# Optimization experiments

Measured on AMD Instinct MI355X. Metric: run time of the kernel, lower is better.

The kernel has to match this reference:

```python
import jax, jax.numpy as jnp
import numpy as np

T, B, IN, H, L = 512, 32, 320, 1024, 3
SLOPE, OFFSET = 0.2, 0.5
FORGET_BIAS = 1.0


def setup_inputs() -> dict:
    key = jax.random.key(0)
    ks = iter(jax.random.split(key, 64))
    stdv = 1.0 / np.sqrt(H)

    def u(k, shape):
        return jax.random.uniform(k, shape, jnp.float32, -stdv, stdv)

    inp = {
        "x": jax.random.normal(next(ks), (T, B, IN), jnp.float32),
        "h0": jnp.zeros((2 * L, B, H), jnp.float32),
        "c0": jnp.zeros((2 * L, B, H), jnp.float32),
    }
    for l in range(L):
        isz = IN if l == 0 else 2 * H
        for d in ("f", "r"):
            inp[f"w_ih_{l}{d}"] = u(next(ks), (4 * H, isz))
            inp[f"w_hh_{l}{d}"] = u(next(ks), (4 * H, H))
            b_ih = u(next(ks), (4 * H,))
            # forget_gate_bias: bias_ih forget slice set, bias_hh forget slice zeroed
            b_ih = b_ih.at[H:2 * H].set(FORGET_BIAS)
            b_hh = u(next(ks), (4 * H,))
            b_hh = b_hh.at[H:2 * H].set(0.0)
            inp[f"b_ih_{l}{d}"] = b_ih
            inp[f"b_hh_{l}{d}"] = b_hh
    return inp


def _hard_lstm_scan(x_seq, h, c, w_ih, w_hh, b):
    """x_seq: [T,B,I]; h,c: [B,H]. Returns ys [T,B,H], (h,c)."""
    # Batch the input-to-hidden GEMM across all timesteps.
    gx = jnp.einsum("tbi,gi->tbg", x_seq, w_ih) + b  # [T,B,4H]

    def step(carry, gxt):
        h, c = carry
        g = gxt + h @ w_hh.T
        i, f, gg, o = jnp.split(g, 4, axis=-1)
        i = jnp.clip(SLOPE * i + OFFSET, 0.0, 1.0)
        f = jnp.clip(SLOPE * f + OFFSET, 0.0, 1.0)
        gg = jnp.clip(gg, -1.0, 1.0)        # hardtanh
        o = jnp.clip(SLOPE * o + OFFSET, 0.0, 1.0)
        c = f * c + i * gg
        h = o * jnp.clip(c, -1.0, 1.0)
        return (h, c), h

    (h, c), ys = jax.lax.scan(step, (h, c), gx)
    return ys, h, c


def hard_lstm_forward(x, h0, c0, params):
    """params: list of L tuples ((fwd 4-tuple), (rev 4-tuple))."""
    y = x
    for l, (pf, pr) in enumerate(params):
        w_ih_f, w_hh_f, b_ih_f, b_hh_f = pf
        w_ih_r, w_hh_r, b_ih_r, b_hh_r = pr
        yf, _, _ = _hard_lstm_scan(y, h0[2 * l], c0[2 * l], w_ih_f, w_hh_f, b_ih_f + b_hh_f)
        yr, _, _ = _hard_lstm_scan(y[::-1], h0[2 * l + 1], c0[2 * l + 1], w_ih_r, w_hh_r, b_ih_r + b_hh_r)
        y = jnp.concatenate([yf, yr[::-1]], axis=-1)  # [T,B,2H]
    return y


def reference(x, h0, c0,
              w_ih_0f, w_hh_0f, b_ih_0f, b_hh_0f,
              w_ih_0r, w_hh_0r, b_ih_0r, b_hh_0r,
              w_ih_1f, w_hh_1f, b_ih_1f, b_hh_1f,
              w_ih_1r, w_hh_1r, b_ih_1r, b_hh_1r,
              w_ih_2f, w_hh_2f, b_ih_2f, b_hh_2f,
              w_ih_2r, w_hh_2r, b_ih_2r, b_hh_2r):
    params = [
        ((w_ih_0f, w_hh_0f, b_ih_0f, b_hh_0f), (w_ih_0r, w_hh_0r, b_ih_0r, b_hh_0r)),
        ((w_ih_1f, w_hh_1f, b_ih_1f, b_hh_1f), (w_ih_1r, w_hh_1r, b_ih_1r, b_hh_1r)),
        ((w_ih_2f, w_hh_2f, b_ih_2f, b_hh_2f), (w_ih_2r, w_hh_2r, b_ih_2r, b_hh_2r)),
    ]
    return hard_lstm_forward(x, h0, c0, params)
```

## Files before the change

kernel.cpp:

```cpp
#include <hip/hip_runtime.h>

typedef __attribute__((ext_vector_type(8))) short short8;
typedef __attribute__((ext_vector_type(4))) short short4v;
typedef __attribute__((ext_vector_type(4))) float f32x4;

__device__ __forceinline__ short f2bf(float x) {
  union { float f; unsigned u; } v; v.f = x;
  unsigned r = v.u + 0x7fffu + ((v.u >> 16) & 1u);
  return (short)(r >> 16);
}
__device__ __forceinline__ float bf2f(short b) {
  union { unsigned u; float f; } v; v.u = ((unsigned)(unsigned short)b) << 16;
  return v.f;
}

#define GLOAD_LDS16(g, l) __builtin_amdgcn_global_load_lds( \
    (const __attribute__((address_space(1))) void*)(g),     \
    (__attribute__((address_space(3))) void*)(l), 16, 0, 0)

__global__ void k_cvt(const float* __restrict__ s, short* __restrict__ d, int n) {
  int stride = gridDim.x * blockDim.x * 4;
  for (int i = (blockIdx.x * blockDim.x + threadIdx.x) * 4; i < n; i += stride) {
    float4 v = *(const float4*)(s + i);
    short4v o;
    o.x = f2bf(v.x); o.y = f2bf(v.y); o.z = f2bf(v.z); o.w = f2bf(v.w);
    *(short4v*)(d + i) = o;
  }
}

__global__ void k_bias(const float* __restrict__ bif, const float* __restrict__ bhf,
                       const float* __restrict__ bir, const float* __restrict__ bhr,
                       float* __restrict__ o) {
  int i = blockIdx.x * 256 + threadIdx.x;
  o[i] = (i < 4096) ? (bif[i] + bhf[i]) : (bir[i - 4096] + bhr[i - 4096]);
}

__global__ void k_zero(int* __restrict__ p) { p[blockIdx.x * 256 + threadIdx.x] = 0; }

__global__ void __launch_bounds__(256) k_gemm(
    const short* __restrict__ A, const short* __restrict__ Bt,
    const float* __restrict__ bias, short* __restrict__ C,
    int M, int N, int K)
{
  __shared__ short Al[128 * 64];
  __shared__ short Bl[128 * 64];
  const int nm = M >> 7;
  int wg = blockIdx.x;
  int q = gridDim.x >> 3;
  wg = (wg & 7) * q + (wg >> 3);
  const int mt = wg % nm, nt = wg / nm;
  const int tid = threadIdx.x, lane = tid & 63, w = tid >> 6;
  const int wr = w >> 1, wc = w & 1;
  const short* Ab = A + (size_t)(mt * 128) * K;
  const short* Bb = Bt + (size_t)(nt * 128) * K;
  f32x4 acc[4][4] = {};
  const int lrow = lane >> 3, lseg = lane & 7;

  for (int kt = 0; kt < K; kt += 64) {
#pragma unroll
    for (int s = 0; s < 4; ++s) {
      int chunk = s * 4 + w;
      int r = chunk * 8 + lrow;
      GLOAD_LDS16(Ab + (size_t)r * K + kt + lseg * 8, &Al[chunk * 512]);
      GLOAD_LDS16(Bb + (size_t)r * K + kt + lseg * 8, &Bl[chunk * 512]);
    }
    __syncthreads();
#pragma unroll
    for (int kk = 0; kk < 2; ++kk) {
      short8 af[4], bfr[4];
#pragma unroll
      for (int i = 0; i < 4; ++i) {
        af[i]  = *(const short8*)&Al[(wr * 64 + i * 16 + (lane & 15)) * 64 + kk * 32 + (lane >> 4) * 8];
        bfr[i] = *(const short8*)&Bl[(wc * 64 + i * 16 + (lane & 15)) * 64 + kk * 32 + (lane >> 4) * 8];
      }
#pragma unroll
      for (int i = 0; i < 4; ++i)
#pragma unroll
        for (int j = 0; j < 4; ++j)
          acc[i][j] = __builtin_amdgcn_mfma_f32_16x16x32_bf16(af[i], bfr[j], acc[i][j], 0, 0, 0);
    }
    __syncthreads();
  }

  const int r0 = mt * 128 + wr * 64, c0n = nt * 128 + wc * 64;
#pragma unroll
  for (int i = 0; i < 4; ++i) {
#pragma unroll
    for (int j = 0; j < 4; ++j) {
      int col = c0n + j * 16 + (lane & 15);
      float bv = bias[col];
#pragma unroll
      for (int r = 0; r < 4; ++r) {
        int row = r0 + i * 16 + (lane >> 4) * 4 + r;
        C[(size_t)row * N + col] = f2bf(acc[i][j][r] + bv);
      }
    }
  }
}

__device__ __forceinline__ void seqwait_slice(int* seqbase, int target, int kq, int lane) {
  if (lane < 32) {
    int* sp = seqbase + (kq * 32 + lane) * 32;
    while (__hip_atomic_load(sp, __ATOMIC_RELAXED, __HIP_MEMORY_SCOPE_AGENT) < target)
      __builtin_amdgcn_s_sleep(1);
  }
  asm volatile("" ::: "memory");
}

template <bool LAST>
__global__ void __launch_bounds__(256, 1) k_scan(
    const short* __restrict__ gx,
    const short* __restrict__ whh,
    const float* __restrict__ h0,
    const float* __restrict__ c0,
    short* __restrict__ hbuf,
    void* __restrict__ yout,
    int layer, int* __restrict__ bar)
{
  const int tid = threadIdx.x, lane = tid & 63, kq = tid >> 6;
  const int dir = blockIdx.x >> 7, wid = blockIdx.x & 127;
  const int hc0 = wid * 8;
  __shared__ float part[4][32][35];
  int* seq = bar + dir * 128 * 32;

  short8 wfr[16];
#pragma unroll
  for (int ni = 0; ni < 2; ++ni) {
    const int lcol = ni * 16 + (lane & 15);
    const int grow = dir * 4096 + (lcol >> 3) * 1024 + hc0 + (lcol & 7);
    const short* wp = whh + (size_t)grow * 1024 + kq * 256 + (lane >> 4) * 8;
#pragma unroll
    for (int ks = 0; ks < 8; ++ks) wfr[ni * 8 + ks] = *(const short8*)(wp + ks * 32);
  }
#pragma unroll
  for (int i = 0; i < 16; ++i) asm volatile("" : "+v"(wfr[i]));

  const int b4 = tid >> 1, cg = tid & 1, col0 = hc0 + cg * 4;
  float ca[4] = {0.f, 0.f, 0.f, 0.f};
  short4v pgi, pgf, pgg, pgo;
  if (tid < 64) {
    const int sidx = ((2 * layer + dir) * 32 + b4) * 1024 + col0;
    float4 cv = *(const float4*)(c0 + sidx);
    ca[0] = cv.x; ca[1] = cv.y; ca[2] = cv.z; ca[3] = cv.w;
    float4 hv = *(const float4*)(h0 + sidx);
    union { unsigned long long u; short s[4]; } pk;
    pk.s[0] = f2bf(hv.x); pk.s[1] = f2bf(hv.y); pk.s[2] = f2bf(hv.z); pk.s[3] = f2bf(hv.w);
    size_t qi = (((size_t)dir * 32 + b4) * 1024 + col0) >> 2;
    __hip_atomic_store((unsigned long long*)hbuf + qi, pk.u,
                       __ATOMIC_RELAXED, __HIP_MEMORY_SCOPE_AGENT);
    asm volatile("s_waitcnt vmcnt(0)" ::: "memory");
  }
  if (tid == 0)
    __hip_atomic_store(seq + wid * 32, 1, __ATOMIC_RELAXED, __HIP_MEMORY_SCOPE_AGENT);
  if (tid < 64) {
    const int t0 = dir ? 511 : 0;
    const short* gp = gx + ((size_t)(t0 * 32 + b4)) * 8192 + dir * 4096 + col0;
    pgi = *(const short4v*)(gp);
    pgf = *(const short4v*)(gp + 1024);
    pgg = *(const short4v*)(gp + 2048);
    pgo = *(const short4v*)(gp + 3072);
  }
  const int arow = lane & 15;
  const int kw = (lane >> 4) * 2;

  int p = 0;
  for (int ts = 0; ts < 512; ++ts) {
    const int t = dir ? (511 - ts) : ts;

    seqwait_slice(seq, ts + 1, kq, lane);
    __syncthreads();

    unsigned long long* hb = (unsigned long long*)hbuf + (size_t)(p * 2 + dir) * 8192;
    short8 af[16];
#pragma unroll
    for (int mi = 0; mi < 2; ++mi) {
      const size_t rb = (size_t)(mi * 16 + arow) * 256 + kq * 64 + kw;
#pragma unroll
      for (int ks = 0; ks < 8; ++ks) {
        union { unsigned long long u[2]; short8 v; } tu;
        tu.u[0] = __hip_atomic_load(hb + rb + ks * 8,     __ATOMIC_RELAXED, __HIP_MEMORY_SCOPE_AGENT);
        tu.u[1] = __hip_atomic_load(hb + rb + ks * 8 + 1, __ATOMIC_RELAXED, __HIP_MEMORY_SCOPE_AGENT);
        af[mi * 8 + ks] = tu.v;
      }
    }
#pragma unroll
    for (int i = 0; i < 16; ++i) asm volatile("" : "+v"(af[i]));

    f32x4 acc[2][2] = {};
#pragma unroll
    for (int ks = 0; ks < 8; ++ks) {
      acc[0][0] = __builtin_amdgcn_mfma_f32_16x16x32_bf16(af[ks],     wfr[ks],     acc[0][0], 0, 0, 0);
      acc[1][0] = __builtin_amdgcn_mfma_f32_16x16x32_bf16(af[8 + ks], wfr[ks],     acc[1][0], 0, 0, 0);
      acc[0][1] = __builtin_amdgcn_mfma_f32_16x16x32_bf16(af[ks],     wfr[8 + ks], acc[0][1], 0, 0, 0);
      acc[1][1] = __builtin_amdgcn_mfma_f32_16x16x32_bf16(af[8 + ks], wfr[8 + ks], acc[1][1], 0, 0, 0);
    }
#pragma unroll
    for (int mi = 0; mi < 2; ++mi)
#pragma unroll
      for (int ni = 0; ni < 2; ++ni)
#pragma unroll
        for (int r = 0; r < 4; ++r)
          part[kq][ni * 16 + (lane & 15)][mi * 16 + (lane >> 4) * 4 + r] = acc[mi][ni][r];
    __syncthreads();

    if (tid < 64) {
      const int c7 = cg * 4;
      float hv[4];
      union { unsigned long long u; short s[4]; } pk;
#pragma unroll
      for (int j = 0; j < 4; ++j) {
        float gi = part[0][c7 + j][b4]      + part[1][c7 + j][b4]      + part[2][c7 + j][b4]      + part[3][c7 + j][b4]      + bf2f(pgi[j]);
        float gf = part[0][8 + c7 + j][b4]  + part[1][8 + c7 + j][b4]  + part[2][8 + c7 + j][b4]  + part[3][8 + c7 + j][b4]  + bf2f(pgf[j]);
        float gg = part[0][16 + c7 + j][b4] + part[1][16 + c7 + j][b4] + part[2][16 + c7 + j][b4] + part[3][16 + c7 + j][b4] + bf2f(pgg[j]);
        float go = part[0][24 + c7 + j][b4] + part[1][24 + c7 + j][b4] + part[2][24 + c7 + j][b4] + part[3][24 + c7 + j][b4] + bf2f(pgo[j]);
        float i_ = fminf(fmaxf(0.2f * gi + 0.5f, 0.f), 1.f);
        float f_ = fminf(fmaxf(0.2f * gf + 0.5f, 0.f), 1.f);
        float g_ = fminf(fmaxf(gg, -1.f), 1.f);
        float o_ = fminf(fmaxf(0.2f * go + 0.5f, 0.f), 1.f);
        float cc = f_ * ca[j] + i_ * g_;
        ca[j] = cc;
        hv[j] = o_ * fminf(fmaxf(cc, -1.f), 1.f);
        pk.s[j] = f2bf(hv[j]);
      }
      size_t qi = (((size_t)((p ^ 1) * 2 + dir) * 32 + b4) * 1024 + col0) >> 2;
      __hip_atomic_store((unsigned long long*)hbuf + qi, pk.u,
                         __ATOMIC_RELAXED, __HIP_MEMORY_SCOPE_AGENT);
      asm volatile("s_waitcnt vmcnt(0)" ::: "memory");
      if (tid == 0)
        __hip_atomic_store(seq + wid * 32, ts + 2, __ATOMIC_RELAXED, __HIP_MEMORY_SCOPE_AGENT);
      size_t yi = ((size_t)(t * 32 + b4)) * 2048 + dir * 1024 + col0;
      if (LAST) {
        float4 f4; f4.x = hv[0]; f4.y = hv[1]; f4.z = hv[2]; f4.w = hv[3];
        *(float4*)((float*)yout + yi) = f4;
      } else {
        short4v ys; ys.x = pk.s[0]; ys.y = pk.s[1]; ys.z = pk.s[2]; ys.w = pk.s[3];
        *(short4v*)((short*)yout + yi) = ys;
      }
      if (ts < 511) {
        const int tn = dir ? (511 - (ts + 1)) : (ts + 1);
        const short* gp = gx + ((size_t)(tn * 32 + b4)) * 8192 + dir * 4096 + col0;
        pgi = *(const short4v*)(gp);
        pgf = *(const short4v*)(gp + 1024);
        pgg = *(const short4v*)(gp + 2048);
        pgo = *(const short4v*)(gp + 3072);
      }
    }
    p ^= 1;
  }
}

extern "C" void kernel_launch(void* const* d_in, const int* in_sizes, int n_in,
                              void* d_out, int out_size, void* d_ws, size_t ws_size,
                              hipStream_t stream)
{
  const float* x  = (const float*)d_in[0];
  const float* h0 = (const float*)d_in[1];
  const float* c0 = (const float*)d_in[2];
  auto W = [&](int l, int d, int k) { return (const float*)d_in[3 + l * 8 + d * 4 + k]; };

  char* base = (char*)d_ws;
  size_t off = 0;
  auto alloc = [&](size_t bytes) {
    void* p = base + off;
    off = (off + bytes + 255) & ~(size_t)255;
    return p;
  };
  short* xb    = (short*)alloc(16384ull * 320 * 2);
  short* wih0  = (short*)alloc(8192ull * 320 * 2);
  short* wih1  = (short*)alloc(8192ull * 2048 * 2);
  short* wih2  = (short*)alloc(8192ull * 2048 * 2);
  short* whh0  = (short*)alloc(8192ull * 1024 * 2);
  short* whh1  = (short*)alloc(8192ull * 1024 * 2);
  short* whh2  = (short*)alloc(8192ull * 1024 * 2);
  float* bias0 = (float*)alloc(8192ull * 4);
  float* bias1 = (float*)alloc(8192ull * 4);
  float* bias2 = (float*)alloc(8192ull * 4);
  short* gx    = (short*)alloc(16384ull * 8192 * 2);
  short* y1    = (short*)alloc(16384ull * 2048 * 2);
  short* y2    = (short*)alloc(16384ull * 2048 * 2);
  short* hbuf  = (short*)alloc(2ull * 2 * 32 * 1024 * 2);
  int*   bar   = (int*)alloc(2ull * 128 * 32 * 4);
  (void)ws_size; (void)in_sizes; (void)n_in; (void)out_size;

  auto cvt = [&](const float* s, short* d, size_t n) {
    size_t want = (n / 4 + 255) / 256;
    int blocks = (int)(want > 2048 ? 2048 : want);
    k_cvt<<<dim3(blocks), dim3(256), 0, stream>>>(s, d, (int)n);
  };

  cvt(x, xb, 16384ull * 320);
  short* wihs[3] = { wih0, wih1, wih2 };
  short* whhs[3] = { whh0, whh1, whh2 };
  float* biases[3] = { bias0, bias1, bias2 };
  for (int l = 0; l < 3; ++l) {
    size_t kin = (l == 0) ? 320 : 2048;
    cvt(W(l, 0, 0), wihs[l],                  4096 * kin);
    cvt(W(l, 1, 0), wihs[l] + 4096 * kin,     4096 * kin);
    cvt(W(l, 0, 1), whhs[l],                  4096ull * 1024);
    cvt(W(l, 1, 1), whhs[l] + 4096ull * 1024, 4096ull * 1024);
    k_bias<<<dim3(32), dim3(256), 0, stream>>>(W(l, 0, 2), W(l, 0, 3), W(l, 1, 2), W(l, 1, 3), biases[l]);
  }

  const int M = 16384, N = 8192;

  k_gemm<<<dim3((M / 128) * (N / 128)), dim3(256), 0, stream>>>(xb, wih0, bias0, gx, M, N, 320);
  k_zero<<<dim3(32), dim3(256), 0, stream>>>(bar);
  {
    const short* gxc = gx; const short* whhc = whh0; short* hb = hbuf;
    void* yo = (void*)y1; int layer = 0;
    void* args[] = { &gxc, &whhc, &h0, &c0, &hb, &yo, &layer, &bar };
    hipLaunchCooperativeKernel(k_scan<false>, dim3(256), dim3(256), args, 0, stream);
  }
  k_gemm<<<dim3((M / 128) * (N / 128)), dim3(256), 0, stream>>>(y1, wih1, bias1, gx, M, N, 2048);
  k_zero<<<dim3(32), dim3(256), 0, stream>>>(bar);
  {
    const short* gxc = gx; const short* whhc = whh1; short* hb = hbuf;
    void* yo = (void*)y2; int layer = 1;
    void* args[] = { &gxc, &whhc, &h0, &c0, &hb, &yo, &layer, &bar };
    hipLaunchCooperativeKernel(k_scan<false>, dim3(256), dim3(256), args, 0, stream);
  }
  k_gemm<<<dim3((M / 128) * (N / 128)), dim3(256), 0, stream>>>(y2, wih2, bias2, gx, M, N, 2048);
  k_zero<<<dim3(32), dim3(256), 0, stream>>>(bar);
  {
    const short* gxc = gx; const short* whhc = whh2; short* hb = hbuf;
    void* yo = d_out; int layer = 2;
    void* args[] = { &gxc, &whhc, &h0, &c0, &hb, &yo, &layer, &bar };
    hipLaunchCooperativeKernel(k_scan<true>, dim3(256), dim3(256), args, 0, stream);
  }
}
```

Measured before the change: 12.09 ms.

## Repartition recurrent scan to 128 blocks of 512 threads with 16 hidden columns each

The persistent LSTM scan now runs on 128 workgroups of 8 waves instead of 256 workgroups of 4 waves. Each block owns 16 hidden columns and splits K across 8 waves, with 128 elementwise threads per block. Each wave now polls only 8 sequence flags instead of 32, which cuts the cross-block synchronisation fan-in per step. The cooperative launch is replaced by a plain launch with dynamic LDS, so co-residency of all blocks is no longer guaranteed by the API. The block also pays an extra __syncthreads per step and a larger LDS reduction.

```diff
diff --git a/kernel.cpp b/kernel.cpp
--- a/kernel.cpp
+++ b/kernel.cpp
@@ -3,6 +3,7 @@
 typedef __attribute__((ext_vector_type(8))) short short8;
 typedef __attribute__((ext_vector_type(4))) short short4v;
 typedef __attribute__((ext_vector_type(4))) float f32x4;
+typedef unsigned long long u64;
 
 __device__ __forceinline__ short f2bf(float x) {
   union { float f; unsigned u; } v; v.f = x;
@@ -98,17 +99,8 @@
   }
 }
 
-__device__ __forceinline__ void seqwait_slice(int* seqbase, int target, int kq, int lane) {
-  if (lane < 32) {
-    int* sp = seqbase + (kq * 32 + lane) * 32;
-    while (__hip_atomic_load(sp, __ATOMIC_RELAXED, __HIP_MEMORY_SCOPE_AGENT) < target)
-      __builtin_amdgcn_s_sleep(1);
-  }
-  asm volatile("" ::: "memory");
-}
-
 template <bool LAST>
-__global__ void __launch_bounds__(256, 1) k_scan(
+__global__ void __launch_bounds__(512, 1) k_scan(
     const short* __restrict__ gx,
     const short* __restrict__ whh,
     const float* __restrict__ h0,
@@ -118,41 +110,42 @@
     int layer, int* __restrict__ bar)
 {
   const int tid = threadIdx.x, lane = tid & 63, kq = tid >> 6;
-  const int dir = blockIdx.x >> 7, wid = blockIdx.x & 127;
-  const int hc0 = wid * 8;
-  __shared__ float part[4][32][35];
-  int* seq = bar + dir * 128 * 32;
+  const int dir = blockIdx.x >> 6, wid = blockIdx.x & 63;
+  const int hc0 = wid * 16;
+  extern __shared__ float part[];
+  int* seq = bar + dir * 64 * 32;
 
   short8 wfr[16];
 #pragma unroll
-  for (int ni = 0; ni < 2; ++ni) {
-    const int lcol = ni * 16 + (lane & 15);
-    const int grow = dir * 4096 + (lcol >> 3) * 1024 + hc0 + (lcol & 7);
-    const short* wp = whh + (size_t)grow * 1024 + kq * 256 + (lane >> 4) * 8;
-#pragma unroll
-    for (int ks = 0; ks < 8; ++ks) wfr[ni * 8 + ks] = *(const short8*)(wp + ks * 32);
+  for (int ni = 0; ni < 4; ++ni) {
+    const int l15 = lane & 15;
+    const int grow = dir * 4096 + ni * 1024 + hc0 + l15;
+    const short* wp = whh + (size_t)grow * 1024 + kq * 128 + (lane >> 4) * 8;
+#pragma unroll
+    for (int ks = 0; ks < 4; ++ks) wfr[ni * 4 + ks] = *(const short8*)(wp + ks * 32);
   }
 #pragma unroll
   for (int i = 0; i < 16; ++i) asm volatile("" : "+v"(wfr[i]));
 
-  const int b4 = tid >> 1, cg = tid & 1, col0 = hc0 + cg * 4;
+  const int b4 = tid >> 2, cg = tid & 3, col0 = hc0 + cg * 4;
   float ca[4] = {0.f, 0.f, 0.f, 0.f};
   short4v pgi, pgf, pgg, pgo;
-  if (tid < 64) {
+  if (tid < 128) {
     const int sidx = ((2 * layer + dir) * 32 + b4) * 1024 + col0;
     float4 cv = *(const float4*)(c0 + sidx);
     ca[0] = cv.x; ca[1] = cv.y; ca[2] = cv.z; ca[3] = cv.w;
     float4 hv = *(const float4*)(h0 + sidx);
-    union { unsigned long long u; short s[4]; } pk;
+    union { u64 u; short s[4]; } pk;
     pk.s[0] = f2bf(hv.x); pk.s[1] = f2bf(hv.y); pk.s[2] = f2bf(hv.z); pk.s[3] = f2bf(hv.w);
-    size_t qi = (((size_t)dir * 32 + b4) * 1024 + col0) >> 2;
-    __hip_atomic_store((unsigned long long*)hbuf + qi, pk.u,
+    size_t qi = (size_t)dir * 8192 + (size_t)b4 * 256 + wid * 4 + cg;
+    __hip_atomic_store((u64*)hbuf + qi, pk.u,
                        __ATOMIC_RELAXED, __HIP_MEMORY_SCOPE_AGENT);
     asm volatile("s_waitcnt vmcnt(0)" ::: "memory");
   }
+  __syncthreads();
   if (tid == 0)
     __hip_atomic_store(seq + wid * 32, 1, __ATOMIC_RELAXED, __HIP_MEMORY_SCOPE_AGENT);
-  if (tid < 64) {
+  if (tid < 128) {
     const int t0 = dir ? 511 : 0;
     const short* gp = gx + ((size_t)(t0 * 32 + b4)) * 8192 + dir * 4096 + col0;
     pgi = *(const short4v*)(gp);
@@ -160,59 +153,68 @@
     pgg = *(const short4v*)(gp + 2048);
     pgo = *(const short4v*)(gp + 3072);
   }
-  const int arow = lane & 15;
-  const int kw = (lane >> 4) * 2;
 
   int p = 0;
   for (int ts = 0; ts < 512; ++ts) {
     const int t = dir ? (511 - ts) : ts;
 
-    seqwait_slice(seq, ts + 1, kq, lane);
-    __syncthreads();
-
-    unsigned long long* hb = (unsigned long long*)hbuf + (size_t)(p * 2 + dir) * 8192;
-    short8 af[16];
+    if (lane < 8) {
+      int* sp = seq + (kq * 8 + lane) * 32;
+      while (__hip_atomic_load(sp, __ATOMIC_RELAXED, __HIP_MEMORY_SCOPE_AGENT) < ts + 1)
+        __builtin_amdgcn_s_sleep(1);
+    }
+    asm volatile("" ::: "memory");
+    __syncthreads();
+
+    u64* hb = (u64*)hbuf + (size_t)(p * 2 + dir) * 8192;
+    short8 af[8];
 #pragma unroll
     for (int mi = 0; mi < 2; ++mi) {
-      const size_t rb = (size_t)(mi * 16 + arow) * 256 + kq * 64 + kw;
-#pragma unroll
-      for (int ks = 0; ks < 8; ++ks) {
-        union { unsigned long long u[2]; short8 v; } tu;
+      const size_t rb = (size_t)(mi * 16 + (lane & 15)) * 256 + kq * 32 + (lane >> 4) * 2;
+#pragma unroll
+      for (int ks = 0; ks < 4; ++ks) {
+        union { u64 u[2]; short8 v; } tu;
         tu.u[0] = __hip_atomic_load(hb + rb + ks * 8,     __ATOMIC_RELAXED, __HIP_MEMORY_SCOPE_AGENT);
         tu.u[1] = __hip_atomic_load(hb + rb + ks * 8 + 1, __ATOMIC_RELAXED, __HIP_MEMORY_SCOPE_AGENT);
-        af[mi * 8 + ks] = tu.v;
-      }
-    }
-#pragma unroll
-    for (int i = 0; i < 16; ++i) asm volatile("" : "+v"(af[i]));
-
-    f32x4 acc[2][2] = {};
-#pragma unroll
-    for (int ks = 0; ks < 8; ++ks) {
-      acc[0][0] = __builtin_amdgcn_mfma_f32_16x16x32_bf16(af[ks],     wfr[ks],     acc[0][0], 0, 0, 0);
-      acc[1][0] = __builtin_amdgcn_mfma_f32_16x16x32_bf16(af[8 + ks], wfr[ks],     acc[1][0], 0, 0, 0);
-      acc[0][1] = __builtin_amdgcn_mfma_f32_16x16x32_bf16(af[ks],     wfr[8 + ks], acc[0][1], 0, 0, 0);
-      acc[1][1] = __builtin_amdgcn_mfma_f32_16x16x32_bf16(af[8 + ks], wfr[8 + ks], acc[1][1], 0, 0, 0);
+        af[mi * 4 + ks] = tu.v;
+      }
+    }
+#pragma unroll
+    for (int i = 0; i < 8; ++i) asm volatile("" : "+v"(af[i]));
+
+    f32x4 acc[2][4] = {};
+#pragma unroll
+    for (int ks = 0; ks < 4; ++ks) {
+#pragma unroll
+      for (int mi = 0; mi < 2; ++mi)
+#pragma unroll
+        for (int ni = 0; ni < 4; ++ni)
+          acc[mi][ni] = __builtin_amdgcn_mfma_f32_16x16x32_bf16(
+              af[mi * 4 + ks], wfr[ni * 4 + ks], acc[mi][ni], 0, 0, 0);
     }
 #pragma unroll
     for (int mi = 0; mi < 2; ++mi)
 #pragma unroll
-      for (int ni = 0; ni < 2; ++ni)
+      for (int ni = 0; ni < 4; ++ni)
 #pragma unroll
         for (int r = 0; r < 4; ++r)
-          part[kq][ni * 16 + (lane & 15)][mi * 16 + (lane >> 4) * 4 + r] = acc[mi][ni][r];
-    __syncthreads();
-
-    if (tid < 64) {
+          part[(kq * 64 + ni * 16 + (lane & 15)) * 35 + mi * 16 + (lane >> 4) * 4 + r] = acc[mi][ni][r];
+    __syncthreads();
+
+    union { u64 u; short s[4]; } pk;
+    float hv[4];
+    if (tid < 128) {
       const int c7 = cg * 4;
-      float hv[4];
-      union { unsigned long long u; short s[4]; } pk;
 #pragma unroll
       for (int j = 0; j < 4; ++j) {
-        float gi = part[0][c7 + j][b4]      + part[1][c7 + j][b4]      + part[2][c7 + j][b4]      + part[3][c7 + j][b4]      + bf2f(pgi[j]);
-        float gf = part[0][8 + c7 + j][b4]  + part[1][8 + c7 + j][b4]  + part[2][8 + c7 + j][b4]  + part[3][8 + c7 + j][b4]  + bf2f(pgf[j]);
-        float gg = part[0][16 + c7 + j][b4] + part[1][16 + c7 + j][b4] + part[2][16 + c7 + j][b4] + part[3][16 + c7 + j][b4] + bf2f(pgg[j]);
-        float go = part[0][24 + c7 + j][b4] + part[1][24 + c7 + j][b4] + part[2][24 + c7 + j][b4] + part[3][24 + c7 + j][b4] + bf2f(pgo[j]);
+        float gi = bf2f(pgi[j]), gf = bf2f(pgf[j]), gg = bf2f(pgg[j]), go = bf2f(pgo[j]);
+#pragma unroll
+        for (int q = 0; q < 8; ++q) {
+          gi += part[(q * 64      + c7 + j) * 35 + b4];
+          gf += part[(q * 64 + 16 + c7 + j) * 35 + b4];
+          gg += part[(q * 64 + 32 + c7 + j) * 35 + b4];
+          go += part[(q * 64 + 48 + c7 + j) * 35 + b4];
+        }
         float i_ = fminf(fmaxf(0.2f * gi + 0.5f, 0.f), 1.f);
         float f_ = fminf(fmaxf(0.2f * gf + 0.5f, 0.f), 1.f);
         float g_ = fminf(fmaxf(gg, -1.f), 1.f);
@@ -222,12 +224,15 @@
         hv[j] = o_ * fminf(fmaxf(cc, -1.f), 1.f);
         pk.s[j] = f2bf(hv[j]);
       }
-      size_t qi = (((size_t)((p ^ 1) * 2 + dir) * 32 + b4) * 1024 + col0) >> 2;
-      __hip_atomic_store((unsigned long long*)hbuf + qi, pk.u,
+      size_t qi = (size_t)((p ^ 1) * 2 + dir) * 8192 + (size_t)b4 * 256 + wid * 4 + cg;
+      __hip_atomic_store((u64*)hbuf + qi, pk.u,
                          __ATOMIC_RELAXED, __HIP_MEMORY_SCOPE_AGENT);
       asm volatile("s_waitcnt vmcnt(0)" ::: "memory");
-      if (tid == 0)
-        __hip_atomic_store(seq + wid * 32, ts + 2, __ATOMIC_RELAXED, __HIP_MEMORY_SCOPE_AGENT);
+    }
+    __syncthreads();
+    if (tid == 0)
+      __hip_atomic_store(seq + wid * 32, ts + 2, __ATOMIC_RELAXED, __HIP_MEMORY_SCOPE_AGENT);
+    if (tid < 128) {
       size_t yi = ((size_t)(t * 32 + b4)) * 2048 + dir * 1024 + col0;
       if (LAST) {
         float4 f4; f4.x = hv[0]; f4.y = hv[1]; f4.z = hv[2]; f4.w = hv[3];
@@ -279,7 +284,7 @@
   short* y1    = (short*)alloc(16384ull * 2048 * 2);
   short* y2    = (short*)alloc(16384ull * 2048 * 2);
   short* hbuf  = (short*)alloc(2ull * 2 * 32 * 1024 * 2);
-  int*   bar   = (int*)alloc(2ull * 128 * 32 * 4);
+  int*   bar   = (int*)alloc(2ull * 64 * 32 * 4);
   (void)ws_size; (void)in_sizes; (void)n_in; (void)out_size;
 
   auto cvt = [&](const float* s, short* d, size_t n) {
@@ -302,29 +307,15 @@
   }
 
   const int M = 16384, N = 8192;
+  const int LDSB = 8 * 64 * 35 * 4;
 
   k_gemm<<<dim3((M / 128) * (N / 128)), dim3(256), 0, stream>>>(xb, wih0, bias0, gx, M, N, 320);
-  k_zero<<<dim3(32), dim3(256), 0, stream>>>(bar);
-  {
-    const short* gxc = gx; const short* whhc = whh0; short* hb = hbuf;
-    void* yo = (void*)y1; int layer = 0;
-    void* args[] = { &gxc, &whhc, &h0, &c0, &hb, &yo, &layer, &bar };
-    hipLaunchCooperativeKernel(k_scan<false>, dim3(256), dim3(256), args, 0, stream);
-  }
+  k_zero<<<dim3(16), dim3(256), 0, stream>>>(bar);
+  k_scan<false><<<dim3(128), dim3(512), LDSB, stream>>>(gx, whh0, h0, c0, hbuf, (void*)y1, 0, bar);
   k_gemm<<<dim3((M / 128) * (N / 128)), dim3(256), 0, stream>>>(y1, wih1, bias1, gx, M, N, 2048);
-  k_zero<<<dim3(32), dim3(256), 0, stream>>>(bar);
-  {
-    const short* gxc = gx; const short* whhc = whh1; short* hb = hbuf;
-    void* yo = (void*)y2; int layer = 1;
-    void* args[] = { &gxc, &whhc, &h0, &c0, &hb, &yo, &layer, &bar };
-    hipLaunchCooperativeKernel(k_scan<false>, dim3(256), dim3(256), args, 0, stream);
-  }
+  k_zero<<<dim3(16), dim3(256), 0, stream>>>(bar);
+  k_scan<false><<<dim3(128), dim3(512), LDSB, stream>>>(gx, whh1, h0, c0, hbuf, (void*)y2, 1, bar);
   k_gemm<<<dim3((M / 128) * (N / 128)), dim3(256), 0, stream>>>(y2, wih2, bias2, gx, M, N, 2048);
-  k_zero<<<dim3(32), dim3(256), 0, stream>>>(bar);
-  {
-    const short* gxc = gx; const short* whhc = whh2; short* hb = hbuf;
-    void* yo = d_out; int layer = 2;
-    void* args[] = { &gxc, &whhc, &h0, &c0, &hb, &yo, &layer, &bar };
-    hipLaunchCooperativeKernel(k_scan<true>, dim3(256), dim3(256), args, 0, stream);
-  }
-}
+  k_zero<<<dim3(16), dim3(256), 0, stream>>>(bar);
+  k_scan<true><<<dim3(128), dim3(512), LDSB, stream>>>(gx, whh2, h0, c0, hbuf, d_out, 2, bar);
+}
```

Result: no change. 11.99 ms (-0.8%).
